# Kernel optimization log

Hardware: AMD Instinct MI355X
Metric: run time of the kernel (lower is better)

## Reference

```python
import jax, jax.numpy as jnp
import numpy as np


def setup_inputs() -> dict:
    key = jax.random.key(0)
    k1, = jax.random.split(key, 1)
    x = jax.random.normal(k1, (16, 512, 64, 64), dtype=jnp.float32)
    gamma = jnp.zeros((1,), dtype=jnp.float32)
    return {"x": x, "gamma": gamma}


def reference(x, gamma):
    B, C, H, W = x.shape
    q = x.reshape(B, C, H * W)              # B x C x N
    # energy: B x C x C  (channel-channel gram matrix)
    energy = jnp.einsum('bcn,bdn->bcd', q, q)
    # max-subtract transform: max over last dim minus energy
    energy_new = jnp.max(energy, axis=-1, keepdims=True) - energy
    attention = jax.nn.softmax(energy_new, axis=-1)  # B x C x C
    out = jnp.einsum('bcd,bdn->bcn', attention, q).reshape(B, C, H, W)
    return gamma * out + x
```

## Files before the change

kernel.cpp:

```cpp
#include <hip/hip_runtime.h>
#include <stdint.h>

#define B_ 16
#define C_ 512
#define N_ 4096

typedef float f32x4 __attribute__((ext_vector_type(4)));
typedef __bf16 bf16x8 __attribute__((ext_vector_type(8)));

static __device__ __forceinline__ unsigned short f2bf(float f) {
    unsigned int u = __float_as_uint(f);
    u += 0x7fffu + ((u >> 16) & 1u);
    return (unsigned short)(u >> 16);
}

static __device__ __forceinline__ void gload_lds16(const void* g, void* l) {
    __builtin_amdgcn_global_load_lds(
        (__attribute__((address_space(1))) unsigned int*)(g),
        (__attribute__((address_space(3))) unsigned int*)(l),
        16, 0, 0);
}

__global__ __launch_bounds__(256)
void convert_transpose(const float* __restrict__ x,
                       unsigned short* __restrict__ q16,
                       unsigned short* __restrict__ qt16) {
    __shared__ unsigned short tile[64][72];
    int b  = blockIdx.z;
    int c0 = blockIdx.y * 64, n0 = blockIdx.x * 64;
    int tx = threadIdx.x & 15, ty = threadIdx.x >> 4;

    const float*    xb  = x    + ((size_t)b * C_ + c0) * N_ + n0;
    unsigned short* qb  = q16  + ((size_t)b * C_ + c0) * N_ + n0;
    unsigned short* qtb = qt16 + ((size_t)b * N_ + n0) * C_ + c0;

#pragma unroll
    for (int s = 0; s < 4; ++s) {
        int rr = s * 16 + ty;
        float4 v = *(const float4*)(xb + (size_t)rr * N_ + tx * 4);
        unsigned short h0 = f2bf(v.x), h1 = f2bf(v.y), h2 = f2bf(v.z), h3 = f2bf(v.w);
        tile[rr][tx * 4 + 0] = h0;
        tile[rr][tx * 4 + 1] = h1;
        tile[rr][tx * 4 + 2] = h2;
        tile[rr][tx * 4 + 3] = h3;
        ushort4 p; p.x = h0; p.y = h1; p.z = h2; p.w = h3;
        *(ushort4*)(qb + (size_t)rr * N_ + tx * 4) = p;
    }
    __syncthreads();
#pragma unroll
    for (int s = 0; s < 4; ++s) {
        int nr = s * 16 + ty;
        ushort4 p;
        p.x = tile[tx * 4 + 0][nr];
        p.y = tile[tx * 4 + 1][nr];
        p.z = tile[tx * 4 + 2][nr];
        p.w = tile[tx * 4 + 3][nr];
        *(ushort4*)(qtb + (size_t)nr * C_ + tx * 4) = p;
    }
}

template<int K>
__global__ __launch_bounds__(256)
void gemm_bt_energy(const unsigned short* __restrict__ q16,
                    float* __restrict__ energy) {
    int b = blockIdx.z;
    const unsigned short* Ab = q16 + (size_t)b * C_ * K;
    const unsigned short* Bb = Ab;
    int m0 = blockIdx.y * 128, n0 = blockIdx.x * 128;

    __shared__ unsigned short As[128 * 32];
    __shared__ unsigned short Bs[128 * 32];

    int t = threadIdx.x;
    int lane = t & 63, wave = t >> 6;
    int wm = (wave >> 1) * 64, wn = (wave & 1) * 64;
    int qd = lane >> 4, r = lane & 15;

    f32x4 acc[4][4] = {};

    for (int k0 = 0; k0 < K; k0 += 32) {
        __syncthreads();
#pragma unroll
        for (int i = 0; i < 2; ++i) {
            int o = (i * 256 + t) * 16;
            int mrow = o >> 6, inrow = o & 63;
            gload_lds16((const char*)Ab + (size_t)(m0 + mrow) * (K * 2) + k0 * 2 + inrow,
                        (char*)As + o);
            gload_lds16((const char*)Bb + (size_t)(n0 + mrow) * (K * 2) + k0 * 2 + inrow,
                        (char*)Bs + o);
        }
        __syncthreads();

        bf16x8 af[4], bfr[4];
#pragma unroll
        for (int i = 0; i < 4; ++i)
            af[i] = *(const bf16x8*)&As[(wm + i * 16 + r) * 32 + qd * 8];
#pragma unroll
        for (int j = 0; j < 4; ++j)
            bfr[j] = *(const bf16x8*)&Bs[(wn + j * 16 + r) * 32 + qd * 8];
#pragma unroll
        for (int i = 0; i < 4; ++i)
#pragma unroll
            for (int j = 0; j < 4; ++j)
                acc[i][j] = __builtin_amdgcn_mfma_f32_16x16x32_bf16(af[i], bfr[j], acc[i][j], 0, 0, 0);
    }

    float* Db = energy + (size_t)b * C_ * C_;
#pragma unroll
    for (int i = 0; i < 4; ++i)
#pragma unroll
        for (int j = 0; j < 4; ++j) {
            int row = m0 + wm + i * 16 + qd * 4;
            int col = n0 + wn + j * 16 + r;
#pragma unroll
            for (int rr = 0; rr < 4; ++rr)
                Db[(size_t)(row + rr) * C_ + col] = acc[i][j][rr];
        }
}

__global__ __launch_bounds__(256)
void softmax_neg(const float* __restrict__ energy, unsigned short* __restrict__ att) {
    size_t row = blockIdx.x;
    const float* e = energy + row * C_;
    int t = threadIdx.x;

    float e0 = e[t], e1 = e[t + 256];
    float m = fminf(e0, e1);
#pragma unroll
    for (int off = 32; off > 0; off >>= 1) m = fminf(m, __shfl_down(m, off, 64));
    __shared__ float red[8];
    if ((t & 63) == 0) red[t >> 6] = m;
    __syncthreads();
    m = fminf(fminf(red[0], red[1]), fminf(red[2], red[3]));

    float p0 = __expf(m - e0), p1 = __expf(m - e1);
    float s = p0 + p1;
#pragma unroll
    for (int off = 32; off > 0; off >>= 1) s += __shfl_down(s, off, 64);
    if ((t & 63) == 0) red[4 + (t >> 6)] = s;
    __syncthreads();
    s = red[4] + red[5] + red[6] + red[7];
    float inv = 1.0f / s;

    att[row * C_ + t]       = f2bf(p0 * inv);
    att[row * C_ + t + 256] = f2bf(p1 * inv);
}

__global__ __launch_bounds__(256)
void gemm_bt_out(const unsigned short* __restrict__ att,
                 const unsigned short* __restrict__ qt16,
                 const float* __restrict__ x,
                 const float* __restrict__ gamma,
                 float* __restrict__ y) {
    const int K = 512;
    int b = blockIdx.z;
    const unsigned short* Ab = att  + (size_t)b * C_ * K;
    const unsigned short* Bb = qt16 + (size_t)b * N_ * K;
    int m0 = blockIdx.y * 128;
    int n0 = blockIdx.x * 128;

    __shared__ unsigned short As[128 * 32];
    __shared__ unsigned short Bs[128 * 32];

    int t = threadIdx.x;
    int lane = t & 63, wave = t >> 6;
    int wm = (wave >> 1) * 64, wn = (wave & 1) * 64;
    int qd = lane >> 4, r = lane & 15;

    f32x4 acc[4][4] = {};

    for (int k0 = 0; k0 < K; k0 += 32) {
        __syncthreads();
#pragma unroll
        for (int i = 0; i < 2; ++i) {
            int o = (i * 256 + t) * 16;
            int mrow = o >> 6, inrow = o & 63;
            gload_lds16((const char*)Ab + (size_t)(m0 + mrow) * (K * 2) + k0 * 2 + inrow,
                        (char*)As + o);
            gload_lds16((const char*)Bb + (size_t)(n0 + mrow) * (K * 2) + k0 * 2 + inrow,
                        (char*)Bs + o);
        }
        __syncthreads();

        bf16x8 af[4], bfr[4];
#pragma unroll
        for (int i = 0; i < 4; ++i)
            af[i] = *(const bf16x8*)&As[(wm + i * 16 + r) * 32 + qd * 8];
#pragma unroll
        for (int j = 0; j < 4; ++j)
            bfr[j] = *(const bf16x8*)&Bs[(wn + j * 16 + r) * 32 + qd * 8];
#pragma unroll
        for (int i = 0; i < 4; ++i)
#pragma unroll
            for (int j = 0; j < 4; ++j)
                acc[i][j] = __builtin_amdgcn_mfma_f32_16x16x32_bf16(af[i], bfr[j], acc[i][j], 0, 0, 0);
    }

    float g = gamma[0];
    const float* xb = x + (size_t)b * C_ * N_;
    float*       yb = y + (size_t)b * C_ * N_;
#pragma unroll
    for (int i = 0; i < 4; ++i)
#pragma unroll
        for (int j = 0; j < 4; ++j) {
            int row = m0 + wm + i * 16 + qd * 4;
            int col = n0 + wn + j * 16 + r;
#pragma unroll
            for (int rr = 0; rr < 4; ++rr) {
                size_t idx = (size_t)(row + rr) * N_ + col;
                yb[idx] = g * acc[i][j][rr] + xb[idx];
            }
        }
}

extern "C" void kernel_launch(void* const* d_in, const int* in_sizes, int n_in,
                              void* d_out, int out_size, void* d_ws, size_t ws_size,
                              hipStream_t stream) {
    const float* x     = (const float*)d_in[0];
    const float* gamma = (const float*)d_in[1];
    float*       y     = (float*)d_out;

    char* ws = (char*)d_ws;
    unsigned short* q16   = (unsigned short*)(ws);
    unsigned short* qt16  = (unsigned short*)(ws + 67108864);
    unsigned short* att16 = (unsigned short*)(ws + 134217728);
    float*          energy= (float*)(ws + 142606336);

    convert_transpose<<<dim3(N_ / 64, C_ / 64, B_), dim3(256), 0, stream>>>(x, q16, qt16);
    gemm_bt_energy<N_><<<dim3(C_ / 128, C_ / 128, B_), dim3(256), 0, stream>>>(q16, energy);
    softmax_neg<<<dim3(B_ * C_), dim3(256), 0, stream>>>(energy, att16);
    gemm_bt_out<<<dim3(N_ / 128, C_ / 128, B_), dim3(256), 0, stream>>>(att16, qt16, x, gamma, y);
}
```

Measured before the change: 419.3 us.

## Triple-buffer GEMM loads, split-K energy GEMM, register-transpose convert kernel

```diff
diff --git a/kernel.cpp b/kernel.cpp
--- a/kernel.cpp
+++ b/kernel.cpp
@@ -21,55 +21,61 @@
         16, 0, 0);
 }
 
+static __device__ __forceinline__ void stage_pair(const char* Ab, const char* Bb,
+                                                  char* as, char* bs, int tid,
+                                                  int rowBytes, int m0, int n0, int kByte) {
+#pragma unroll
+    for (int i = 0; i < 2; ++i) {
+        int o = (i * 256 + tid) * 16;
+        int mrow = o >> 6, inrow = o & 63;
+        gload_lds16(Ab + (size_t)(m0 + mrow) * rowBytes + kByte + inrow, as + o);
+        gload_lds16(Bb + (size_t)(n0 + mrow) * rowBytes + kByte + inrow, bs + o);
+    }
+}
+
 __global__ __launch_bounds__(256)
 void convert_transpose(const float* __restrict__ x,
                        unsigned short* __restrict__ q16,
                        unsigned short* __restrict__ qt16) {
-    __shared__ unsigned short tile[64][72];
-    int b  = blockIdx.z;
-    int c0 = blockIdx.y * 64, n0 = blockIdx.x * 64;
-    int tx = threadIdx.x & 15, ty = threadIdx.x >> 4;
-
-    const float*    xb  = x    + ((size_t)b * C_ + c0) * N_ + n0;
-    unsigned short* qb  = q16  + ((size_t)b * C_ + c0) * N_ + n0;
+    int b = blockIdx.z;
+    int t = threadIdx.x;
+    int c0 = blockIdx.y * 64 + (t >> 4) * 4;
+    int n0 = blockIdx.x * 64 + (t & 15) * 4;
+
+    const float* xb = x + ((size_t)b * C_ + c0) * N_ + n0;
+    unsigned short h[4][4];
+#pragma unroll
+    for (int i = 0; i < 4; ++i) {
+        float4 v = *(const float4*)(xb + (size_t)i * N_);
+        h[i][0] = f2bf(v.x); h[i][1] = f2bf(v.y);
+        h[i][2] = f2bf(v.z); h[i][3] = f2bf(v.w);
+    }
+    unsigned short* qb = q16 + ((size_t)b * C_ + c0) * N_ + n0;
+#pragma unroll
+    for (int i = 0; i < 4; ++i) {
+        ushort4 p; p.x = h[i][0]; p.y = h[i][1]; p.z = h[i][2]; p.w = h[i][3];
+        *(ushort4*)(qb + (size_t)i * N_) = p;
+    }
     unsigned short* qtb = qt16 + ((size_t)b * N_ + n0) * C_ + c0;
-
-#pragma unroll
-    for (int s = 0; s < 4; ++s) {
-        int rr = s * 16 + ty;
-        float4 v = *(const float4*)(xb + (size_t)rr * N_ + tx * 4);
-        unsigned short h0 = f2bf(v.x), h1 = f2bf(v.y), h2 = f2bf(v.z), h3 = f2bf(v.w);
-        tile[rr][tx * 4 + 0] = h0;
-        tile[rr][tx * 4 + 1] = h1;
-        tile[rr][tx * 4 + 2] = h2;
-        tile[rr][tx * 4 + 3] = h3;
-        ushort4 p; p.x = h0; p.y = h1; p.z = h2; p.w = h3;
-        *(ushort4*)(qb + (size_t)rr * N_ + tx * 4) = p;
-    }
-    __syncthreads();
-#pragma unroll
-    for (int s = 0; s < 4; ++s) {
-        int nr = s * 16 + ty;
-        ushort4 p;
-        p.x = tile[tx * 4 + 0][nr];
-        p.y = tile[tx * 4 + 1][nr];
-        p.z = tile[tx * 4 + 2][nr];
-        p.w = tile[tx * 4 + 3][nr];
-        *(ushort4*)(qtb + (size_t)nr * C_ + tx * 4) = p;
-    }
-}
-
-template<int K>
+#pragma unroll
+    for (int j = 0; j < 4; ++j) {
+        ushort4 p; p.x = h[0][j]; p.y = h[1][j]; p.z = h[2][j]; p.w = h[3][j];
+        *(ushort4*)(qtb + (size_t)j * C_) = p;
+    }
+}
+
+template<int KROW, int NT>
 __global__ __launch_bounds__(256)
 void gemm_bt_energy(const unsigned short* __restrict__ q16,
-                    float* __restrict__ energy) {
-    int b = blockIdx.z;
-    const unsigned short* Ab = q16 + (size_t)b * C_ * K;
-    const unsigned short* Bb = Ab;
+                    float* __restrict__ e0, float* __restrict__ e1) {
+    int zb = blockIdx.z;
+    int b = zb >> 1, ks = zb & 1;
+    int kbeg = ks * (NT * 32);
+    const char* Ab = (const char*)(q16 + (size_t)b * C_ * KROW);
     int m0 = blockIdx.y * 128, n0 = blockIdx.x * 128;
 
-    __shared__ unsigned short As[128 * 32];
-    __shared__ unsigned short Bs[128 * 32];
+    __shared__ unsigned short As[3][128 * 32];
+    __shared__ unsigned short Bs[3][128 * 32];
 
     int t = threadIdx.x;
     int lane = t & 63, wave = t >> 6;
@@ -78,34 +84,44 @@
 
     f32x4 acc[4][4] = {};
 
-    for (int k0 = 0; k0 < K; k0 += 32) {
-        __syncthreads();
-#pragma unroll
-        for (int i = 0; i < 2; ++i) {
-            int o = (i * 256 + t) * 16;
-            int mrow = o >> 6, inrow = o & 63;
-            gload_lds16((const char*)Ab + (size_t)(m0 + mrow) * (K * 2) + k0 * 2 + inrow,
-                        (char*)As + o);
-            gload_lds16((const char*)Bb + (size_t)(n0 + mrow) * (K * 2) + k0 * 2 + inrow,
-                        (char*)Bs + o);
-        }
-        __syncthreads();
-
+    const int rowB = KROW * 2;
+    stage_pair(Ab, Ab, (char*)As[0], (char*)Bs[0], t, rowB, m0, n0, kbeg * 2);
+    stage_pair(Ab, Ab, (char*)As[1], (char*)Bs[1], t, rowB, m0, n0, (kbeg + 32) * 2);
+
+    int bufi = 0;
+    for (int tt = 0; tt < NT; ++tt) {
+        if (tt < NT - 1) asm volatile("s_waitcnt vmcnt(4) lgkmcnt(0)" ::: "memory");
+        else             asm volatile("s_waitcnt vmcnt(0) lgkmcnt(0)" ::: "memory");
+        __builtin_amdgcn_s_barrier();
+
+        if (tt + 2 < NT) {
+            int nb = bufi + 2; if (nb >= 3) nb -= 3;
+            stage_pair(Ab, Ab, (char*)As[nb], (char*)Bs[nb], t, rowB,
+                       m0, n0, (kbeg + (tt + 2) * 32) * 2);
+        }
+
+        const unsigned short* as = As[bufi];
+        const unsigned short* bs = Bs[bufi];
         bf16x8 af[4], bfr[4];
 #pragma unroll
         for (int i = 0; i < 4; ++i)
-            af[i] = *(const bf16x8*)&As[(wm + i * 16 + r) * 32 + qd * 8];
+            af[i] = *(const bf16x8*)&as[(wm + i * 16 + r) * 32 + qd * 8];
 #pragma unroll
         for (int j = 0; j < 4; ++j)
-            bfr[j] = *(const bf16x8*)&Bs[(wn + j * 16 + r) * 32 + qd * 8];
+            bfr[j] = *(const bf16x8*)&bs[(wn + j * 16 + r) * 32 + qd * 8];
+
+        __builtin_amdgcn_s_setprio(1);
 #pragma unroll
         for (int i = 0; i < 4; ++i)
 #pragma unroll
             for (int j = 0; j < 4; ++j)
                 acc[i][j] = __builtin_amdgcn_mfma_f32_16x16x32_bf16(af[i], bfr[j], acc[i][j], 0, 0, 0);
-    }
-
-    float* Db = energy + (size_t)b * C_ * C_;
+        __builtin_amdgcn_s_setprio(0);
+
+        if (++bufi == 3) bufi = 0;
+    }
+
+    float* Db = (ks ? e1 : e0) + (size_t)b * C_ * C_;
 #pragma unroll
     for (int i = 0; i < 4; ++i)
 #pragma unroll
@@ -119,13 +135,15 @@
 }
 
 __global__ __launch_bounds__(256)
-void softmax_neg(const float* __restrict__ energy, unsigned short* __restrict__ att) {
+void softmax_neg(const float* __restrict__ e0, const float* __restrict__ e1,
+                 unsigned short* __restrict__ att) {
     size_t row = blockIdx.x;
-    const float* e = energy + row * C_;
-    int t = threadIdx.x;
-
-    float e0 = e[t], e1 = e[t + 256];
-    float m = fminf(e0, e1);
+    const float* a = e0 + row * C_;
+    const float* c = e1 + row * C_;
+    int t = threadIdx.x;
+
+    float x0 = a[t] + c[t], x1 = a[t + 256] + c[t + 256];
+    float m = fminf(x0, x1);
 #pragma unroll
     for (int off = 32; off > 0; off >>= 1) m = fminf(m, __shfl_down(m, off, 64));
     __shared__ float red[8];
@@ -133,7 +151,7 @@
     __syncthreads();
     m = fminf(fminf(red[0], red[1]), fminf(red[2], red[3]));
 
-    float p0 = __expf(m - e0), p1 = __expf(m - e1);
+    float p0 = __expf(m - x0), p1 = __expf(m - x1);
     float s = p0 + p1;
 #pragma unroll
     for (int off = 32; off > 0; off >>= 1) s += __shfl_down(s, off, 64);
@@ -153,14 +171,15 @@
                  const float* __restrict__ gamma,
                  float* __restrict__ y) {
     const int K = 512;
+    const int NT = K / 32;
     int b = blockIdx.z;
-    const unsigned short* Ab = att  + (size_t)b * C_ * K;
-    const unsigned short* Bb = qt16 + (size_t)b * N_ * K;
+    const char* Ab = (const char*)(att  + (size_t)b * C_ * K);
+    const char* Bb = (const char*)(qt16 + (size_t)b * N_ * K);
     int m0 = blockIdx.y * 128;
     int n0 = blockIdx.x * 128;
 
-    __shared__ unsigned short As[128 * 32];
-    __shared__ unsigned short Bs[128 * 32];
+    __shared__ unsigned short As[3][128 * 32];
+    __shared__ unsigned short Bs[3][128 * 32];
 
     int t = threadIdx.x;
     int lane = t & 63, wave = t >> 6;
@@ -169,31 +188,41 @@
 
     f32x4 acc[4][4] = {};
 
-    for (int k0 = 0; k0 < K; k0 += 32) {
-        __syncthreads();
-#pragma unroll
-        for (int i = 0; i < 2; ++i) {
-            int o = (i * 256 + t) * 16;
-            int mrow = o >> 6, inrow = o & 63;
-            gload_lds16((const char*)Ab + (size_t)(m0 + mrow) * (K * 2) + k0 * 2 + inrow,
-                        (char*)As + o);
-            gload_lds16((const char*)Bb + (size_t)(n0 + mrow) * (K * 2) + k0 * 2 + inrow,
-                        (char*)Bs + o);
-        }
-        __syncthreads();
-
+    const int rowB = K * 2;
+    stage_pair(Ab, Bb, (char*)As[0], (char*)Bs[0], t, rowB, m0, n0, 0);
+    stage_pair(Ab, Bb, (char*)As[1], (char*)Bs[1], t, rowB, m0, n0, 64);
+
+    int bufi = 0;
+    for (int tt = 0; tt < NT; ++tt) {
+        if (tt < NT - 1) asm volatile("s_waitcnt vmcnt(4) lgkmcnt(0)" ::: "memory");
+        else             asm volatile("s_waitcnt vmcnt(0) lgkmcnt(0)" ::: "memory");
+        __builtin_amdgcn_s_barrier();
+
+        if (tt + 2 < NT) {
+            int nb = bufi + 2; if (nb >= 3) nb -= 3;
+            stage_pair(Ab, Bb, (char*)As[nb], (char*)Bs[nb], t, rowB,
+                       m0, n0, (tt + 2) * 64);
+        }
+
+        const unsigned short* as = As[bufi];
+        const unsigned short* bs = Bs[bufi];
         bf16x8 af[4], bfr[4];
 #pragma unroll
         for (int i = 0; i < 4; ++i)
-            af[i] = *(const bf16x8*)&As[(wm + i * 16 + r) * 32 + qd * 8];
+            af[i] = *(const bf16x8*)&as[(wm + i * 16 + r) * 32 + qd * 8];
 #pragma unroll
         for (int j = 0; j < 4; ++j)
-            bfr[j] = *(const bf16x8*)&Bs[(wn + j * 16 + r) * 32 + qd * 8];
+            bfr[j] = *(const bf16x8*)&bs[(wn + j * 16 + r) * 32 + qd * 8];
+
+        __builtin_amdgcn_s_setprio(1);
 #pragma unroll
         for (int i = 0; i < 4; ++i)
 #pragma unroll
             for (int j = 0; j < 4; ++j)
                 acc[i][j] = __builtin_amdgcn_mfma_f32_16x16x32_bf16(af[i], bfr[j], acc[i][j], 0, 0, 0);
+        __builtin_amdgcn_s_setprio(0);
+
+        if (++bufi == 3) bufi = 0;
     }
 
     float g = gamma[0];
@@ -221,13 +250,14 @@
     float*       y     = (float*)d_out;
 
     char* ws = (char*)d_ws;
-    unsigned short* q16   = (unsigned short*)(ws);
-    unsigned short* qt16  = (unsigned short*)(ws + 67108864);
-    unsigned short* att16 = (unsigned short*)(ws + 134217728);
-    float*          energy= (float*)(ws + 142606336);
+    unsigned short* q16    = (unsigned short*)(ws);
+    unsigned short* qt16   = (unsigned short*)(ws + 67108864);
+    unsigned short* att16  = (unsigned short*)(ws + 134217728);
+    float*          energy0= (float*)(ws + 142606336);
+    float*          energy1= (float*)d_out;
 
     convert_transpose<<<dim3(N_ / 64, C_ / 64, B_), dim3(256), 0, stream>>>(x, q16, qt16);
-    gemm_bt_energy<N_><<<dim3(C_ / 128, C_ / 128, B_), dim3(256), 0, stream>>>(q16, energy);
-    softmax_neg<<<dim3(B_ * C_), dim3(256), 0, stream>>>(energy, att16);
+    gemm_bt_energy<N_, N_ / 64><<<dim3(C_ / 128, C_ / 128, B_ * 2), dim3(256), 0, stream>>>(q16, energy0, energy1);
+    softmax_neg<<<dim3(B_ * C_), dim3(256), 0, stream>>>(energy0, energy1, att16);
     gemm_bt_out<<<dim3(N_ / 128, C_ / 128, B_), dim3(256), 0, stream>>>(att16, qt16, x, gamma, y);
 }
```

Measured after the change: 398.4 us. 1.05x faster.

## Split-K energy GEMM, double-buffer LDS with swizzle, remap block order

Applied to the files above, without the earlier changes.

```diff
diff --git a/kernel.cpp b/kernel.cpp
--- a/kernel.cpp
+++ b/kernel.cpp
@@ -25,7 +25,7 @@
 void convert_transpose(const float* __restrict__ x,
                        unsigned short* __restrict__ q16,
                        unsigned short* __restrict__ qt16) {
-    __shared__ unsigned short tile[64][72];
+    __shared__ unsigned short tile[64][65];
     int b  = blockIdx.z;
     int c0 = blockIdx.y * 64, n0 = blockIdx.x * 64;
     int tx = threadIdx.x & 15, ty = threadIdx.x >> 4;
@@ -59,53 +59,75 @@
     }
 }
 
-template<int K>
-__global__ __launch_bounds__(256)
-void gemm_bt_energy(const unsigned short* __restrict__ q16,
-                    float* __restrict__ energy) {
-    int b = blockIdx.z;
-    const unsigned short* Ab = q16 + (size_t)b * C_ * K;
-    const unsigned short* Bb = Ab;
-    int m0 = blockIdx.y * 128, n0 = blockIdx.x * 128;
-
-    __shared__ unsigned short As[128 * 32];
-    __shared__ unsigned short Bs[128 * 32];
+
+__global__ __launch_bounds__(256, 3)
+void gemm_energy(const unsigned short* __restrict__ q16,
+                 float* __restrict__ e0, float* __restrict__ e1) {
+    int bid = blockIdx.x;
+    int g = bid & 31, tl = bid >> 5;
+    int b = g >> 1, ks = g & 1;
+    int m0 = (tl >> 2) * 128, n0 = (tl & 3) * 128;
+    const int NT = 64;
+    const int rowB = N_ * 2;
+    const char* Ab = (const char*)(q16 + (size_t)b * C_ * N_);
+    int kbegByte = ks * 2048 * 2;
+
+    __shared__ char lds[2][16384];
 
     int t = threadIdx.x;
     int lane = t & 63, wave = t >> 6;
     int wm = (wave >> 1) * 64, wn = (wave & 1) * 64;
     int qd = lane >> 4, r = lane & 15;
 
+    const char* src[4];
+#pragma unroll
+    for (int i = 0; i < 4; ++i) {
+        int v = i * 256 + t;
+        int row = v >> 3, slot = v & 7, code = slot ^ (row & 7);
+        int isB = code >> 2, col = (code & 3) * 16;
+        src[i] = Ab + (size_t)((isB ? n0 : m0) + row) * rowB + kbegByte + col;
+    }
+    int aoff = (wm + r) * 128 + ((qd ^ (r & 7)) << 4);
+    int boff = (wn + r) * 128 + (((4 | qd) ^ (r & 7)) << 4);
+
     f32x4 acc[4][4] = {};
 
-    for (int k0 = 0; k0 < K; k0 += 32) {
-        __syncthreads();
-#pragma unroll
-        for (int i = 0; i < 2; ++i) {
-            int o = (i * 256 + t) * 16;
-            int mrow = o >> 6, inrow = o & 63;
-            gload_lds16((const char*)Ab + (size_t)(m0 + mrow) * (K * 2) + k0 * 2 + inrow,
-                        (char*)As + o);
-            gload_lds16((const char*)Bb + (size_t)(n0 + mrow) * (K * 2) + k0 * 2 + inrow,
-                        (char*)Bs + o);
-        }
-        __syncthreads();
-
+#pragma unroll
+    for (int i = 0; i < 4; ++i) gload_lds16(src[i],      &lds[0][(i * 256 + t) * 16]);
+#pragma unroll
+    for (int i = 0; i < 4; ++i) gload_lds16(src[i] + 64, &lds[1][(i * 256 + t) * 16]);
+
+    for (int tt = 0; tt < NT; ++tt) {
+        if (tt < NT - 1) asm volatile("s_waitcnt vmcnt(4)" ::: "memory");
+        else             asm volatile("s_waitcnt vmcnt(0)" ::: "memory");
+        __builtin_amdgcn_s_barrier();
+
+        const char* base = lds[tt & 1];
         bf16x8 af[4], bfr[4];
 #pragma unroll
-        for (int i = 0; i < 4; ++i)
-            af[i] = *(const bf16x8*)&As[(wm + i * 16 + r) * 32 + qd * 8];
-#pragma unroll
-        for (int j = 0; j < 4; ++j)
-            bfr[j] = *(const bf16x8*)&Bs[(wn + j * 16 + r) * 32 + qd * 8];
+        for (int i = 0; i < 4; ++i) af[i]  = *(const bf16x8*)(base + aoff + i * 2048);
+#pragma unroll
+        for (int j = 0; j < 4; ++j) bfr[j] = *(const bf16x8*)(base + boff + j * 2048);
+        asm volatile("s_waitcnt lgkmcnt(0)" ::: "memory");
+        __builtin_amdgcn_s_barrier();
+
+        if (tt + 2 < NT) {
+            int kB = (tt + 2) * 64;
+            char* d = lds[tt & 1];
+#pragma unroll
+            for (int i = 0; i < 4; ++i) gload_lds16(src[i] + kB, d + (i * 256 + t) * 16);
+        }
+
+        __builtin_amdgcn_s_setprio(1);
 #pragma unroll
         for (int i = 0; i < 4; ++i)
 #pragma unroll
             for (int j = 0; j < 4; ++j)
                 acc[i][j] = __builtin_amdgcn_mfma_f32_16x16x32_bf16(af[i], bfr[j], acc[i][j], 0, 0, 0);
-    }
-
-    float* Db = energy + (size_t)b * C_ * C_;
+        __builtin_amdgcn_s_setprio(0);
+    }
+
+    float* Db = (ks ? e1 : e0) + (size_t)b * C_ * C_;
 #pragma unroll
     for (int i = 0; i < 4; ++i)
 #pragma unroll
@@ -119,13 +141,15 @@
 }
 
 __global__ __launch_bounds__(256)
-void softmax_neg(const float* __restrict__ energy, unsigned short* __restrict__ att) {
+void softmax_neg(const float* __restrict__ e0, const float* __restrict__ e1,
+                 unsigned short* __restrict__ att) {
     size_t row = blockIdx.x;
-    const float* e = energy + row * C_;
+    const float* a = e0 + row * C_;
+    const float* c = e1 + row * C_;
     int t = threadIdx.x;
 
-    float e0 = e[t], e1 = e[t + 256];
-    float m = fminf(e0, e1);
+    float x0 = a[t] + c[t], x1 = a[t + 256] + c[t + 256];
+    float m = fminf(x0, x1);
 #pragma unroll
     for (int off = 32; off > 0; off >>= 1) m = fminf(m, __shfl_down(m, off, 64));
     __shared__ float red[8];
@@ -133,7 +157,7 @@
     __syncthreads();
     m = fminf(fminf(red[0], red[1]), fminf(red[2], red[3]));
 
-    float p0 = __expf(m - e0), p1 = __expf(m - e1);
+    float p0 = __expf(m - x0), p1 = __expf(m - x1);
     float s = p0 + p1;
 #pragma unroll
     for (int off = 32; off > 0; off >>= 1) s += __shfl_down(s, off, 64);
@@ -146,57 +170,80 @@
     att[row * C_ + t + 256] = f2bf(p1 * inv);
 }
 
-__global__ __launch_bounds__(256)
+__global__ __launch_bounds__(256, 3)
 void gemm_bt_out(const unsigned short* __restrict__ att,
                  const unsigned short* __restrict__ qt16,
                  const float* __restrict__ x,
                  const float* __restrict__ gamma,
                  float* __restrict__ y) {
     const int K = 512;
-    int b = blockIdx.z;
-    const unsigned short* Ab = att  + (size_t)b * C_ * K;
-    const unsigned short* Bb = qt16 + (size_t)b * N_ * K;
-    int m0 = blockIdx.y * 128;
-    int n0 = blockIdx.x * 128;
-
-    __shared__ unsigned short As[128 * 32];
-    __shared__ unsigned short Bs[128 * 32];
+    const int NT = K / 32;
+    int bid = blockIdx.x;
+    int g = bid & 127, tl = bid >> 7;
+    int b = g >> 3, nch = g & 7;
+    int m0 = (tl >> 2) * 128;
+    int n0 = (nch * 4 + (tl & 3)) * 128;
+    const int rowB = K * 2;
+    const char* Ab = (const char*)(att  + (size_t)b * C_ * K);
+    const char* Bb = (const char*)(qt16 + (size_t)b * N_ * K);
+
+    __shared__ char lds[2][16384];
 
     int t = threadIdx.x;
     int lane = t & 63, wave = t >> 6;
     int wm = (wave >> 1) * 64, wn = (wave & 1) * 64;
     int qd = lane >> 4, r = lane & 15;
 
+    const char* src[4];
+#pragma unroll
+    for (int i = 0; i < 4; ++i) {
+        int v = i * 256 + t;
+        int row = v >> 3, slot = v & 7, code = slot ^ (row & 7);
+        int isB = code >> 2, col = (code & 3) * 16;
+        src[i] = (isB ? Bb + (size_t)(n0 + row) * rowB
+                      : Ab + (size_t)(m0 + row) * rowB) + col;
+    }
+    int aoff = (wm + r) * 128 + ((qd ^ (r & 7)) << 4);
+    int boff = (wn + r) * 128 + (((4 | qd) ^ (r & 7)) << 4);
+
     f32x4 acc[4][4] = {};
 
-    for (int k0 = 0; k0 < K; k0 += 32) {
-        __syncthreads();
-#pragma unroll
-        for (int i = 0; i < 2; ++i) {
-            int o = (i * 256 + t) * 16;
-            int mrow = o >> 6, inrow = o & 63;
-            gload_lds16((const char*)Ab + (size_t)(m0 + mrow) * (K * 2) + k0 * 2 + inrow,
-                        (char*)As + o);
-            gload_lds16((const char*)Bb + (size_t)(n0 + mrow) * (K * 2) + k0 * 2 + inrow,
-                        (char*)Bs + o);
-        }
-        __syncthreads();
-
+#pragma unroll
+    for (int i = 0; i < 4; ++i) gload_lds16(src[i],      &lds[0][(i * 256 + t) * 16]);
+#pragma unroll
+    for (int i = 0; i < 4; ++i) gload_lds16(src[i] + 64, &lds[1][(i * 256 + t) * 16]);
+
+    for (int tt = 0; tt < NT; ++tt) {
+        if (tt < NT - 1) asm volatile("s_waitcnt vmcnt(4)" ::: "memory");
+        else             asm volatile("s_waitcnt vmcnt(0)" ::: "memory");
+        __builtin_amdgcn_s_barrier();
+
+        const char* base = lds[tt & 1];
         bf16x8 af[4], bfr[4];
 #pragma unroll
-        for (int i = 0; i < 4; ++i)
-            af[i] = *(const bf16x8*)&As[(wm + i * 16 + r) * 32 + qd * 8];
-#pragma unroll
-        for (int j = 0; j < 4; ++j)
-            bfr[j] = *(const bf16x8*)&Bs[(wn + j * 16 + r) * 32 + qd * 8];
+        for (int i = 0; i < 4; ++i) af[i]  = *(const bf16x8*)(base + aoff + i * 2048);
+#pragma unroll
+        for (int j = 0; j < 4; ++j) bfr[j] = *(const bf16x8*)(base + boff + j * 2048);
+        asm volatile("s_waitcnt lgkmcnt(0)" ::: "memory");
+        __builtin_amdgcn_s_barrier();
+
+        if (tt + 2 < NT) {
+            int kB = (tt + 2) * 64;
+            char* d = lds[tt & 1];
+#pragma unroll
+            for (int i = 0; i < 4; ++i) gload_lds16(src[i] + kB, d + (i * 256 + t) * 16);
+        }
+
+        __builtin_amdgcn_s_setprio(1);
 #pragma unroll
         for (int i = 0; i < 4; ++i)
 #pragma unroll
             for (int j = 0; j < 4; ++j)
                 acc[i][j] = __builtin_amdgcn_mfma_f32_16x16x32_bf16(af[i], bfr[j], acc[i][j], 0, 0, 0);
-    }
-
-    float g = gamma[0];
+        __builtin_amdgcn_s_setprio(0);
+    }
+
+    float g_ = gamma[0];
     const float* xb = x + (size_t)b * C_ * N_;
     float*       yb = y + (size_t)b * C_ * N_;
 #pragma unroll
@@ -208,7 +255,7 @@
 #pragma unroll
             for (int rr = 0; rr < 4; ++rr) {
                 size_t idx = (size_t)(row + rr) * N_ + col;
-                yb[idx] = g * acc[i][j][rr] + xb[idx];
+                yb[idx] = g_ * acc[i][j][rr] + xb[idx];
             }
         }
 }
@@ -224,10 +271,11 @@
     unsigned short* q16   = (unsigned short*)(ws);
     unsigned short* qt16  = (unsigned short*)(ws + 67108864);
     unsigned short* att16 = (unsigned short*)(ws + 134217728);
-    float*          energy= (float*)(ws + 142606336);
+    float*          e0    = (float*)(ws + 142606336);
+    float*          e1    = (float*)d_out;
 
     convert_transpose<<<dim3(N_ / 64, C_ / 64, B_), dim3(256), 0, stream>>>(x, q16, qt16);
-    gemm_bt_energy<N_><<<dim3(C_ / 128, C_ / 128, B_), dim3(256), 0, stream>>>(q16, energy);
-    softmax_neg<<<dim3(B_ * C_), dim3(256), 0, stream>>>(energy, att16);
-    gemm_bt_out<<<dim3(N_ / 128, C_ / 128, B_), dim3(256), 0, stream>>>(att16, qt16, x, gamma, y);
-}
+    gemm_energy<<<dim3(512), dim3(256), 0, stream>>>(q16, e0, e1);
+    softmax_neg<<<dim3(B_ * C_), dim3(256), 0, stream>>>(e0, e1, att16);
+    gemm_bt_out<<<dim3(2048), dim3(256), 0, stream>>>(att16, qt16, x, gamma, y);
+}
```

Measured after the change: 388.8 us. 1.08x faster.
